# Kernel optimization log

Measured on AMD Instinct MI355X. Metric: run time of the kernel, lower is better.

Reference implementation:

```python
import math
import jax, jax.numpy as jnp
import numpy as np

B, T, G, E, H, L = 8, 32, 32, 768, 12, 4
S = T * G
HD = E // H


def setup_inputs() -> dict:
    key = jax.random.key(0)
    ks = jax.random.split(key, 10)
    def n(k, shape, s=0.02):
        return s * jax.random.normal(k, shape, jnp.float32)
    return dict(
        x=jax.random.normal(ks[0], (B, T, G, E), jnp.float32),
        study_date=jnp.sort(jax.random.randint(ks[1], (B, T), 0, 50), axis=-1),
        wpe=n(ks[2], (50, E)),
        ln1_w=jnp.ones((L, E)), ln1_b=jnp.zeros((L, E)),
        in_w=n(ks[3], (L, 3 * E, E)), in_b=jnp.zeros((L, 3 * E)),
        out_w=n(ks[4], (L, E, E)), out_b=jnp.zeros((L, E)),
        ln2_w=jnp.ones((L, E)), ln2_b=jnp.zeros((L, E)),
        fc_w=n(ks[5], (L, 4 * E, E)), fc_b=jnp.zeros((L, 4 * E)),
        proj_w=n(ks[6], (L, E, 4 * E), 0.02 / math.sqrt(2 * L)),
        proj_b=jnp.zeros((L, E)),
        lnf_w=jnp.ones((E,)), lnf_b=jnp.zeros((E,)),
    )


def _ln(x, w, b):
    m = x.mean(-1, keepdims=True)
    v = ((x - m) ** 2).mean(-1, keepdims=True)
    return (x - m) / jnp.sqrt(v + 1e-5) * w + b


def _gelu_new(x):
    # NewGELU: 0.5*x*(1+tanh(sqrt(2/pi)*(x+0.044715*x^3)))
    c = np.sqrt(2.0 / np.pi).astype(np.float32)
    return 0.5 * x * (1.0 + jnp.tanh(c * (x + 0.044715 * x ** 3)))


def _mask_bias():
    # block-causal mask: tril over T blocks, each expanded to G x G
    allowed = jnp.tril(jnp.ones((T, T), bool))
    allowed = jnp.repeat(jnp.repeat(allowed, G, axis=0), G, axis=1)  # [S,S]
    return jnp.where(allowed, 0.0, -jnp.inf).astype(jnp.float32)


def reference(x, study_date, wpe, ln1_w, ln1_b, in_w, in_b, out_w, out_b,
              ln2_w, ln2_b, fc_w, fc_b, proj_w, proj_b, lnf_w, lnf_b):
    b, t, g, d = x.shape
    s = t * g
    pos = wpe[jnp.clip(study_date, 0, 49)]  # [B,T,E]
    pos = jnp.broadcast_to(pos[:, :, None, :], (b, t, g, d)).reshape(b, s, d)
    h = x.reshape(b, s, d) + pos
    bias = _mask_bias()  # [S,S]
    inv_sqrt_hd = 1.0 / np.sqrt(HD).astype(np.float32)
    for l in range(L):
        y = _ln(h, ln1_w[l], ln1_b[l])
        qkv = y @ in_w[l].T + in_b[l]  # [B,S,3E]
        q, k, v = jnp.split(qkv, 3, axis=-1)
        q = q.reshape(b, s, H, HD).transpose(0, 2, 1, 3)
        k = k.reshape(b, s, H, HD).transpose(0, 2, 1, 3)
        v = v.reshape(b, s, H, HD).transpose(0, 2, 1, 3)
        att = jnp.einsum('bhqd,bhkd->bhqk', q, k) * inv_sqrt_hd + bias
        att = jax.nn.softmax(att, axis=-1)
        o = jnp.einsum('bhqk,bhkd->bhqd', att, v)
        o = o.transpose(0, 2, 1, 3).reshape(b, s, d)
        h = h + o @ out_w[l].T + out_b[l]
        y2 = _ln(h, ln2_w[l], ln2_b[l])
        h = h + _gelu_new(y2 @ fc_w[l].T + fc_b[l]) @ proj_w[l].T + proj_b[l]
    return _ln(h, lnf_w, lnf_b)
```

## Files before the change

### kernel.cpp

```cpp
#include <hip/hip_runtime.h>
#include <hip/hip_bf16.h>

typedef __attribute__((ext_vector_type(8))) __bf16 bf16x8;
typedef __attribute__((ext_vector_type(4))) float f32x4;

typedef unsigned short u16;
typedef __attribute__((ext_vector_type(8))) u16 u16x8;

__device__ __forceinline__ u16 f2bf(float f) {
    unsigned int u = __float_as_uint(f);
    u += 0x7FFFu + ((u >> 16) & 1u);
    return (u16)(u >> 16);
}

__device__ __forceinline__ void g2l16(const void* g, void* l) {
    __builtin_amdgcn_global_load_lds(
        (const __attribute__((address_space(1))) void*)g,
        (__attribute__((address_space(3))) void*)l, 16, 0, 0);
}

#define BB 8
#define SS 1024
#define EE 768
#define HH 12
#define HD 64
#define LL 4

__global__ __launch_bounds__(256) void cvt_k(const float* __restrict__ in,
                                             u16* __restrict__ out, int n4) {
    for (int i = blockIdx.x * 256 + threadIdx.x; i < n4; i += gridDim.x * 256) {
        float4 v = ((const float4*)in)[i];
        ushort4 u;
        u.x = f2bf(v.x); u.y = f2bf(v.y); u.z = f2bf(v.z); u.w = f2bf(v.w);
        ((ushort4*)out)[i] = u;
    }
}

__global__ __launch_bounds__(256) void embed_k(const float* __restrict__ x,
                                               const int* __restrict__ sd,
                                               const float* __restrict__ wpe,
                                               float* __restrict__ h) {
    int idx = blockIdx.x * 256 + threadIdx.x;
    int e4 = idx % 192;
    int bs = idx / 192;
    int b = bs >> 10;
    int t = (bs >> 5) & 31;
    int date = sd[b * 32 + t];
    date = date < 0 ? 0 : (date > 49 ? 49 : date);
    float4 xv = ((const float4*)x)[idx];
    float4 pv = ((const float4*)wpe)[date * 192 + e4];
    float4 r; r.x = xv.x + pv.x; r.y = xv.y + pv.y; r.z = xv.z + pv.z; r.w = xv.w + pv.w;
    ((float4*)h)[idx] = r;
}

template <bool BF16OUT>
__global__ __launch_bounds__(256) void ln_k(const float* __restrict__ in,
                                            const float* __restrict__ w,
                                            const float* __restrict__ b,
                                            void* __restrict__ out) {
    int tid = threadIdx.x, wv = tid >> 6, lane = tid & 63;
    int token = blockIdx.x * 4 + wv;
    const float4* ip = (const float4*)(in + (size_t)token * EE);
    float4 v[3];
#pragma unroll
    for (int p = 0; p < 3; p++) v[p] = ip[p * 64 + lane];
    float s = 0.f;
#pragma unroll
    for (int p = 0; p < 3; p++) s += v[p].x + v[p].y + v[p].z + v[p].w;
#pragma unroll
    for (int m = 1; m < 64; m <<= 1) s += __shfl_xor(s, m);
    float mean = s * (1.f / 768.f);
    float vs = 0.f;
#pragma unroll
    for (int p = 0; p < 3; p++) {
        float dx = v[p].x - mean, dy = v[p].y - mean, dz = v[p].z - mean, dw = v[p].w - mean;
        vs += dx * dx + dy * dy + dz * dz + dw * dw;
    }
#pragma unroll
    for (int m = 1; m < 64; m <<= 1) vs += __shfl_xor(vs, m);
    float rstd = rsqrtf(vs * (1.f / 768.f) + 1e-5f);
    const float4* wp = (const float4*)w;
    const float4* bp = (const float4*)b;
#pragma unroll
    for (int p = 0; p < 3; p++) {
        float4 wv4 = wp[p * 64 + lane], bv4 = bp[p * 64 + lane];
        float rx = (v[p].x - mean) * rstd * wv4.x + bv4.x;
        float ry = (v[p].y - mean) * rstd * wv4.y + bv4.y;
        float rz = (v[p].z - mean) * rstd * wv4.z + bv4.z;
        float rw = (v[p].w - mean) * rstd * wv4.w + bv4.w;
        if (BF16OUT) {
            ushort4 u; u.x = f2bf(rx); u.y = f2bf(ry); u.z = f2bf(rz); u.w = f2bf(rw);
            ((ushort4*)((u16*)out + (size_t)token * EE))[p * 64 + lane] = u;
        } else {
            float4 r; r.x = rx; r.y = ry; r.z = rz; r.w = rw;
            ((float4*)((float*)out + (size_t)token * EE))[p * 64 + lane] = r;
        }
    }
}

template <int MODE, int BM, int NST>
__global__ __launch_bounds__(256) void gemm_bt(const u16* __restrict__ A,
                                               const u16* __restrict__ Bw,
                                               const float* __restrict__ bias,
                                               float* __restrict__ hres,
                                               u16* __restrict__ outb,
                                               u16* __restrict__ vT,
                                               u16* __restrict__ kT,
                                               int M, int N, int K) {
    constexpr int TM = BM / 32;
    constexpr int PD = NST - 2;
    constexpr int ATILE = BM * 32;
    constexpr int TILE = ATILE + 4096;
    constexpr int SSTR = TILE * 2;
    __shared__ u16 SM[NST * TILE];

    const int tid = threadIdx.x;
    const int lane = tid & 63, w = tid >> 6;
    const int quad = lane >> 4, l16 = lane & 15;

    const int nx = N >> 7;
    const int ny = M / BM;
    const int id = blockIdx.x;
    const int xcd = id & 7, s = id >> 3;
    const int yt = xcd * (ny >> 3) + s / nx;
    const int xt = s % nx;
    const int m0 = yt * BM, n0 = xt * 128;
    const int wm = (w >> 1) * (BM / 2), wn = (w & 1) * 64;

    f32x4 acc[TM][4];
#pragma unroll
    for (int i = 0; i < TM; i++)
#pragma unroll
        for (int j = 0; j < 4; j++) acc[i][j] = (f32x4){0.f, 0.f, 0.f, 0.f};

    const int swz = (quad ^ ((l16 >> 1) & 3)) * 8;
    const int nk = K >> 5;

    const int cB0 = w * 128 + lane, cB1 = cB0 + 64;
    const int rB0 = cB0 >> 2, gB0 = (((cB0 & 3) ^ ((cB0 >> 3) & 3)) * 8);
    const int rB1 = cB1 >> 2, gB1 = (((cB1 & 3) ^ ((cB1 >> 3) & 3)) * 8);
    const u16* Bp0 = Bw + (size_t)(n0 + rB0) * K + gB0;
    const u16* Bp1 = Bw + (size_t)(n0 + rB1) * K + gB1;
    char* lB0 = (char*)SM + ATILE * 2 + w * 2048;
    char* lB1 = lB0 + 1024;
    const int cA0 = (BM == 128) ? cB0 : tid;
    const int rA0 = cA0 >> 2, gA0 = (((cA0 & 3) ^ ((cA0 >> 3) & 3)) * 8);
    const u16* Ap0 = A + (size_t)(m0 + rA0) * K + gA0;
    char* lA0 = (char*)SM + ((BM == 128) ? w * 2048 : w * 1024);
    const int cA1 = cB1;
    const int rA1 = cA1 >> 2, gA1 = (((cA1 & 3) ^ ((cA1 >> 3) & 3)) * 8);
    const u16* Ap1 = A + (size_t)(m0 + rA1) * K + gA1;
    char* lA1 = (char*)SM + w * 2048 + 1024;

#pragma unroll
    for (int p = 0; p < PD; p++) {
        g2l16(Ap0 + p * 32, lA0 + p * SSTR);
        if (BM == 128) g2l16(Ap1 + p * 32, lA1 + p * SSTR);
        g2l16(Bp0 + p * 32, lB0 + p * SSTR);
        g2l16(Bp1 + p * 32, lB1 + p * SSTR);
    }

    int rb = 0, wb = PD;
    for (int ki = 0; ki < nk; ki++) {
        if (ki + PD < nk) {
            const int kb = (ki + PD) << 5;
            const int bo = wb * SSTR;
            g2l16(Ap0 + kb, lA0 + bo);
            if (BM == 128) g2l16(Ap1 + kb, lA1 + bo);
            g2l16(Bp0 + kb, lB0 + bo);
            g2l16(Bp1 + kb, lB1 + bo);
        }
        {
            const int rem = nk - 1 - ki;
            const int d = rem < PD ? rem : PD;
            if (BM == 128) {
                if (PD == 2) {
                    if (d == 2)      __builtin_amdgcn_s_waitcnt(0x0F78);
                    else if (d == 1) __builtin_amdgcn_s_waitcnt(0x0F74);
                    else             __builtin_amdgcn_s_waitcnt(0x0F70);
                } else {
                    if (d == 1)      __builtin_amdgcn_s_waitcnt(0x0F74);
                    else             __builtin_amdgcn_s_waitcnt(0x0F70);
                }
            } else {
                if (d == 2)      __builtin_amdgcn_s_waitcnt(0x0F76);
                else if (d == 1) __builtin_amdgcn_s_waitcnt(0x0F73);
                else             __builtin_amdgcn_s_waitcnt(0x0F70);
            }
        }
        __builtin_amdgcn_s_barrier();

        const u16* Ab = (const u16*)SM + rb * TILE;
        const u16* Bb = Ab + ATILE;
        bf16x8 af[TM], bfr[4];
#pragma unroll
        for (int t = 0; t < TM; t++)
            af[t] = *(const bf16x8*)(Ab + (wm + t * 16 + l16) * 32 + swz);
#pragma unroll
        for (int t = 0; t < 4; t++)
            bfr[t] = *(const bf16x8*)(Bb + (wn + t * 16 + l16) * 32 + swz);
#pragma unroll
        for (int tm = 0; tm < TM; tm++)
#pragma unroll
            for (int tn = 0; tn < 4; tn++)
                acc[tm][tn] = __builtin_amdgcn_mfma_f32_16x16x32_bf16(
                    af[tm], bfr[tn], acc[tm][tn], 0, 0, 0);
        rb = (rb + 1 == NST) ? 0 : rb + 1;
        wb = (wb + 1 == NST) ? 0 : wb + 1;
    }

#pragma unroll
    for (int tm = 0; tm < TM; tm++) {
        int rowm = m0 + wm + tm * 16 + quad * 4;
#pragma unroll
        for (int tn = 0; tn < 4; tn++) {
            int coln = n0 + wn + tn * 16 + l16;
            float bv = bias[coln];
            f32x4 v = acc[tm][tn];
            if (MODE == 0) {
                int b = rowm >> 10, s2 = rowm & 1023;
                if (coln < EE) {
                    int hh = coln >> 6, d = coln & 63;
                    u16* qp = outb + ((size_t)(b * HH + hh) * SS + s2) * HD + d;
#pragma unroll
                    for (int r = 0; r < 4; r++) qp[r * HD] = f2bf(v[r] + bv);
                } else if (coln < 2 * EE) {
                    int hh = (coln - EE) >> 6, d = (coln - EE) & 63;
                    u16* kp = kT + ((size_t)(b * HH + hh) * SS + s2) * HD + d;
#pragma unroll
                    for (int r = 0; r < 4; r++) kp[r * HD] = f2bf(v[r] + bv);
                } else {
                    int hh = (coln - 2 * EE) >> 6, d = (coln - 2 * EE) & 63;
                    int j0 = s2 & 31;
                    int k0 = (j0 < 16) ? ((j0 >> 2) * 8) : (((j0 - 16) >> 2) * 8 + 4);
                    int s2p = (s2 & ~31) | k0;
                    ushort4 pk;
                    pk.x = f2bf(v[0] + bv); pk.y = f2bf(v[1] + bv);
                    pk.z = f2bf(v[2] + bv); pk.w = f2bf(v[3] + bv);
                    *(ushort4*)(vT + (((size_t)((b * HH + hh) * HD + d)) << 10) + s2p) = pk;
                }
            } else if (MODE == 1) {
#pragma unroll
                for (int r = 0; r < 4; r++) {
                    size_t idx = (size_t)(rowm + r) * N + coln;
                    hres[idx] += v[r] + bv;
                }
            } else {
#pragma unroll
                for (int r = 0; r < 4; r++) {
                    float x = v[r] + bv;
                    float t = x + 0.044715f * x * x * x;
                    float e = __expf(-1.5957691216057308f * t);
                    float th = (1.f - e) / (1.f + e);
                    outb[(size_t)(rowm + r) * N + coln] = f2bf(0.5f * x * (1.f + th));
                }
            }
        }
    }
}

__global__ __launch_bounds__(256) void attn_k(const u16* __restrict__ qT,
                                              const u16* __restrict__ kT,
                                              const u16* __restrict__ vT,
                                              u16* __restrict__ o) {
    __shared__ u16 Ks[2048];
    __shared__ u16 Vs[2048];
    int tid = threadIdx.x, w = tid >> 6, lane = tid & 63;
    int quad = lane >> 4, l16 = lane & 15;
    int blk = blockIdx.x;
    int qg = 15 - (blk / 96);
    int bh = blk % 96;
    int b = bh / HH, hh = bh % HH;
    int q0 = qg * 64;
    int kend_blk = q0 + 64;
    int kend_w = q0 + ((w >> 1) ? 64 : 32);

    const u16* qbase = qT + ((size_t)bh * SS + q0 + w * 16 + l16) * HD + quad * 8;
    bf16x8 qf0 = *(const bf16x8*)(qbase);
    bf16x8 qf1 = *(const bf16x8*)(qbase + 32);

    f32x4 of[4];
#pragma unroll
    for (int i = 0; i < 4; i++) of[i] = (f32x4){0.f, 0.f, 0.f, 0.f};
    float mrun = -__builtin_inff(), lrun = 0.f;

    int tK = tid >> 3, dcK = ((tid & 7) ^ (tK & 7));
    const u16* kg = kT + ((size_t)bh * SS + tK) * HD + dcK * 8;
    char* kl = (char*)Ks + w * 1024;
    int dV = tid >> 2, tcV = ((tid & 3) ^ ((dV >> 1) & 3));
    const u16* vg = vT + ((size_t)bh * HD + dV) * SS + tcV * 8;
    char* vl = (char*)Vs + w * 1024;

    for (int kb = 0; kb < kend_blk; kb += 32) {
        g2l16(kg + (size_t)kb * HD, kl);
        g2l16(vg + kb, vl);
        __syncthreads();
        if (kb < kend_w) {
            int t0 = l16, t1 = 16 + l16;
            bf16x8 k00 = *(const bf16x8*)(Ks + (t0 * 8 + (quad ^ (l16 & 7))) * 8);
            bf16x8 k01 = *(const bf16x8*)(Ks + (t0 * 8 + ((4 + quad) ^ (l16 & 7))) * 8);
            bf16x8 k10 = *(const bf16x8*)(Ks + (t1 * 8 + (quad ^ (l16 & 7))) * 8);
            bf16x8 k11 = *(const bf16x8*)(Ks + (t1 * 8 + ((4 + quad) ^ (l16 & 7))) * 8);
            f32x4 sT0 = (f32x4){0.f, 0.f, 0.f, 0.f};
            f32x4 sT1 = (f32x4){0.f, 0.f, 0.f, 0.f};
            sT0 = __builtin_amdgcn_mfma_f32_16x16x32_bf16(k00, qf0, sT0, 0, 0, 0);
            sT0 = __builtin_amdgcn_mfma_f32_16x16x32_bf16(k01, qf1, sT0, 0, 0, 0);
            sT1 = __builtin_amdgcn_mfma_f32_16x16x32_bf16(k10, qf0, sT1, 0, 0, 0);
            sT1 = __builtin_amdgcn_mfma_f32_16x16x32_bf16(k11, qf1, sT1, 0, 0, 0);

            float a0[4], a1[4];
#pragma unroll
            for (int r = 0; r < 4; r++) { a0[r] = sT0[r] * 0.125f; a1[r] = sT1[r] * 0.125f; }
            float mx = fmaxf(fmaxf(fmaxf(a0[0], a0[1]), fmaxf(a0[2], a0[3])),
                             fmaxf(fmaxf(a1[0], a1[1]), fmaxf(a1[2], a1[3])));
            mx = fmaxf(mx, __shfl_xor(mx, 16));
            mx = fmaxf(mx, __shfl_xor(mx, 32));
            if (!__all(mx - mrun <= 8.0f)) {
                float mnew = fmaxf(mrun, mx);
                float alpha = __expf(mrun - mnew);
                mrun = mnew;
                lrun *= alpha;
                float al[4];
#pragma unroll
                for (int r = 0; r < 4; r++) al[r] = __shfl(alpha, quad * 4 + r);
#pragma unroll
                for (int n4 = 0; n4 < 4; n4++) {
                    of[n4][0] *= al[0]; of[n4][1] *= al[1];
                    of[n4][2] *= al[2]; of[n4][3] *= al[3];
                }
            }
            float p0[4], p1[4];
#pragma unroll
            for (int r = 0; r < 4; r++) {
                p0[r] = __expf(a0[r] - mrun);
                p1[r] = __expf(a1[r] - mrun);
            }
            float ps = ((p0[0] + p0[1]) + (p0[2] + p0[3])) +
                       ((p1[0] + p1[1]) + (p1[2] + p1[3]));
            ps += __shfl_xor(ps, 16);
            ps += __shfl_xor(ps, 32);
            lrun += ps;
            union { u16x8 u; bf16x8 v; } pa;
            pa.u[0] = f2bf(p0[0]); pa.u[1] = f2bf(p0[1]);
            pa.u[2] = f2bf(p0[2]); pa.u[3] = f2bf(p0[3]);
            pa.u[4] = f2bf(p1[0]); pa.u[5] = f2bf(p1[1]);
            pa.u[6] = f2bf(p1[2]); pa.u[7] = f2bf(p1[3]);
#pragma unroll
            for (int n4 = 0; n4 < 4; n4++) {
                int d = n4 * 16 + l16;
                bf16x8 vf = *(const bf16x8*)(Vs + (d * 4 + (quad ^ ((d >> 1) & 3))) * 8);
                of[n4] = __builtin_amdgcn_mfma_f32_16x16x32_bf16(pa.v, vf, of[n4], 0, 0, 0);
            }
        }
        __syncthreads();
    }

    float linv[4];
#pragma unroll
    for (int r = 0; r < 4; r++) linv[r] = 1.f / __shfl(lrun, quad * 4 + r);
#pragma unroll
    for (int n4 = 0; n4 < 4; n4++)
#pragma unroll
        for (int r = 0; r < 4; r++)
            o[(size_t)(b * SS + q0 + w * 16 + quad * 4 + r) * EE + hh * HD + n4 * 16 + l16] =
                f2bf(of[n4][r] * linv[r]);
}

extern "C" void kernel_launch(void* const* d_in, const int* in_sizes, int n_in,
                              void* d_out, int out_size, void* d_ws, size_t ws_size,
                              hipStream_t stream) {
    const float* x     = (const float*)d_in[0];
    const int*   sd    = (const int*)d_in[1];
    const float* wpe   = (const float*)d_in[2];
    const float* ln1w  = (const float*)d_in[3];
    const float* ln1b  = (const float*)d_in[4];
    const float* in_w  = (const float*)d_in[5];
    const float* in_b  = (const float*)d_in[6];
    const float* out_w = (const float*)d_in[7];
    const float* out_b = (const float*)d_in[8];
    const float* ln2w  = (const float*)d_in[9];
    const float* ln2b  = (const float*)d_in[10];
    const float* fc_w  = (const float*)d_in[11];
    const float* fc_b  = (const float*)d_in[12];
    const float* pr_w  = (const float*)d_in[13];
    const float* pr_b  = (const float*)d_in[14];
    const float* lnfw  = (const float*)d_in[15];
    const float* lnfb  = (const float*)d_in[16];
    float* outp = (float*)d_out;

    char* ws = (char*)d_ws;
    float* h   = (float*)ws;
    u16* ybuf  = (u16*)(ws + 25165824);
    u16* big   = (u16*)(ws + 37748736);
    u16* qT    = big;
    u16* kT    = big + 6291456;
    u16* vT    = (u16*)(ws + 88080384);
    u16* wb    = (u16*)(ws + 100663296);
    u16* w_in  = wb;
    u16* w_out = w_in + 7077888;
    u16* w_fc  = w_out + 2359296;
    u16* w_pr  = w_fc + 9437184;

    cvt_k<<<1024, 256, 0, stream>>>(in_w,  w_in,  7077888 / 4);
    cvt_k<<<1024, 256, 0, stream>>>(out_w, w_out, 2359296 / 4);
    cvt_k<<<1024, 256, 0, stream>>>(fc_w,  w_fc,  9437184 / 4);
    cvt_k<<<1024, 256, 0, stream>>>(pr_w,  w_pr,  9437184 / 4);
    embed_k<<<6144, 256, 0, stream>>>(x, sd, wpe, h);

    for (int l = 0; l < LL; l++) {
        ln_k<true><<<2048, 256, 0, stream>>>(h, ln1w + l * EE, ln1b + l * EE, ybuf);
        gemm_bt<0, 128, 3><<<18 * 64, 256, 0, stream>>>(
            ybuf, w_in + (size_t)l * 2304 * 768, in_b + l * 2304, nullptr, qT, vT, kT,
            8192, 2304, 768);
        attn_k<<<1536, 256, 0, stream>>>(qT, kT, vT, ybuf);
        gemm_bt<1, 64, 4><<<6 * 128, 256, 0, stream>>>(
            ybuf, w_out + (size_t)l * 768 * 768, out_b + l * 768, h, nullptr, nullptr, nullptr,
            8192, 768, 768);
        ln_k<true><<<2048, 256, 0, stream>>>(h, ln2w + l * EE, ln2b + l * EE, ybuf);
        gemm_bt<2, 128, 3><<<24 * 64, 256, 0, stream>>>(
            ybuf, w_fc + (size_t)l * 3072 * 768, fc_b + l * 3072, nullptr, big, nullptr, nullptr,
            8192, 3072, 768);
        gemm_bt<1, 128, 4><<<6 * 64, 256, 0, stream>>>(
            big, w_pr + (size_t)l * 768 * 3072, pr_b + l * 768, h, nullptr, nullptr, nullptr,
            8192, 768, 3072);
    }
    ln_k<false><<<2048, 256, 0, stream>>>(h, lnfw, lnfb, outp);
}
```

Measured before the change: 1.170 ms.

## Split-K the MLP projection GEMM and fold residual add into LayerNorm

The projection GEMM (K=3072) now runs with split-K of 2, doubling the grid from 384 to 768 blocks to fill more CUs. Each half writes its partial sum as bf16 into a scratch buffer (ybuf or vT) instead of doing a read-modify-write on the fp32 residual. The next LayerNorm (or the final one) loads both partials, adds them to h, writes h back and then normalizes, which fuses the residual update into an existing pass. The cost is that the partial sums are rounded to bf16 before accumulation, which loses some precision, and the pipeline depth drops from 4 to 3 stages.

```diff
diff --git a/kernel.cpp b/kernel.cpp
--- a/kernel.cpp
+++ b/kernel.cpp
@@ -11,6 +11,10 @@
     unsigned int u = __float_as_uint(f);
     u += 0x7FFFu + ((u >> 16) & 1u);
     return (u16)(u >> 16);
+}
+
+__device__ __forceinline__ float b2f(u16 u) {
+    return __uint_as_float((unsigned int)u << 16);
 }
 
 __device__ __forceinline__ void g2l16(const void* g, void* l) {
@@ -53,17 +57,37 @@
     ((float4*)h)[idx] = r;
 }
 
-template <bool BF16OUT>
+template <bool BF16OUT, bool ADDP>
 __global__ __launch_bounds__(256) void ln_k(const float* __restrict__ in,
                                             const float* __restrict__ w,
                                             const float* __restrict__ b,
-                                            void* __restrict__ out) {
+                                            void* __restrict__ out,
+                                            const u16* p0, const u16* p1,
+                                            float* hback) {
     int tid = threadIdx.x, wv = tid >> 6, lane = tid & 63;
     int token = blockIdx.x * 4 + wv;
     const float4* ip = (const float4*)(in + (size_t)token * EE);
     float4 v[3];
 #pragma unroll
     for (int p = 0; p < 3; p++) v[p] = ip[p * 64 + lane];
+    if (ADDP) {
+        const ushort4* q0 = (const ushort4*)(p0 + (size_t)token * EE);
+        const ushort4* q1 = (const ushort4*)(p1 + (size_t)token * EE);
+#pragma unroll
+        for (int p = 0; p < 3; p++) {
+            ushort4 a = q0[p * 64 + lane];
+            ushort4 c = q1[p * 64 + lane];
+            v[p].x += b2f(a.x) + b2f(c.x);
+            v[p].y += b2f(a.y) + b2f(c.y);
+            v[p].z += b2f(a.z) + b2f(c.z);
+            v[p].w += b2f(a.w) + b2f(c.w);
+        }
+        if (hback) {
+            float4* hp = (float4*)(hback + (size_t)token * EE);
+#pragma unroll
+            for (int p = 0; p < 3; p++) hp[p * 64 + lane] = v[p];
+        }
+    }
     float s = 0.f;
 #pragma unroll
     for (int p = 0; p < 3; p++) s += v[p].x + v[p].y + v[p].z + v[p].w;
@@ -98,7 +122,7 @@
     }
 }
 
-template <int MODE, int BM, int NST>
+template <int MODE, int BM, int NST, int SPLITK>
 __global__ __launch_bounds__(256) void gemm_bt(const u16* __restrict__ A,
                                                const u16* __restrict__ Bw,
                                                const float* __restrict__ bias,
@@ -120,12 +144,19 @@
 
     const int nx = N >> 7;
     const int ny = M / BM;
-    const int id = blockIdx.x;
+    int id = blockIdx.x;
+    int ks = 0;
+    if (SPLITK == 2) {
+        const int half = ny * nx;
+        ks = id >= half;
+        id -= ks * half;
+    }
     const int xcd = id & 7, s = id >> 3;
     const int yt = xcd * (ny >> 3) + s / nx;
     const int xt = s % nx;
     const int m0 = yt * BM, n0 = xt * 128;
     const int wm = (w >> 1) * (BM / 2), wn = (w & 1) * 64;
+    const int kbase = ks * (K / SPLITK);
 
     f32x4 acc[TM][4];
 #pragma unroll
@@ -134,22 +165,22 @@
         for (int j = 0; j < 4; j++) acc[i][j] = (f32x4){0.f, 0.f, 0.f, 0.f};
 
     const int swz = (quad ^ ((l16 >> 1) & 3)) * 8;
-    const int nk = K >> 5;
+    const int nk = (K / SPLITK) >> 5;
 
     const int cB0 = w * 128 + lane, cB1 = cB0 + 64;
     const int rB0 = cB0 >> 2, gB0 = (((cB0 & 3) ^ ((cB0 >> 3) & 3)) * 8);
     const int rB1 = cB1 >> 2, gB1 = (((cB1 & 3) ^ ((cB1 >> 3) & 3)) * 8);
-    const u16* Bp0 = Bw + (size_t)(n0 + rB0) * K + gB0;
-    const u16* Bp1 = Bw + (size_t)(n0 + rB1) * K + gB1;
+    const u16* Bp0 = Bw + (size_t)(n0 + rB0) * K + kbase + gB0;
+    const u16* Bp1 = Bw + (size_t)(n0 + rB1) * K + kbase + gB1;
     char* lB0 = (char*)SM + ATILE * 2 + w * 2048;
     char* lB1 = lB0 + 1024;
     const int cA0 = (BM == 128) ? cB0 : tid;
     const int rA0 = cA0 >> 2, gA0 = (((cA0 & 3) ^ ((cA0 >> 3) & 3)) * 8);
-    const u16* Ap0 = A + (size_t)(m0 + rA0) * K + gA0;
+    const u16* Ap0 = A + (size_t)(m0 + rA0) * K + kbase + gA0;
     char* lA0 = (char*)SM + ((BM == 128) ? w * 2048 : w * 1024);
     const int cA1 = cB1;
     const int rA1 = cA1 >> 2, gA1 = (((cA1 & 3) ^ ((cA1 >> 3) & 3)) * 8);
-    const u16* Ap1 = A + (size_t)(m0 + rA1) * K + gA1;
+    const u16* Ap1 = A + (size_t)(m0 + rA1) * K + kbase + gA1;
     char* lA1 = (char*)SM + w * 2048 + 1024;
 
 #pragma unroll
@@ -245,7 +276,7 @@
                     size_t idx = (size_t)(rowm + r) * N + coln;
                     hres[idx] += v[r] + bv;
                 }
-            } else {
+            } else if (MODE == 2) {
 #pragma unroll
                 for (int r = 0; r < 4; r++) {
                     float x = v[r] + bv;
@@ -254,6 +285,12 @@
                     float th = (1.f - e) / (1.f + e);
                     outb[(size_t)(rowm + r) * N + coln] = f2bf(0.5f * x * (1.f + th));
                 }
+            } else {
+                u16* pb = ks ? vT : outb;
+                float badd = ks ? 0.f : bv;
+#pragma unroll
+                for (int r = 0; r < 4; r++)
+                    pb[(size_t)(rowm + r) * N + coln] = f2bf(v[r] + badd);
             }
         }
     }
@@ -408,21 +445,28 @@
     embed_k<<<6144, 256, 0, stream>>>(x, sd, wpe, h);
 
     for (int l = 0; l < LL; l++) {
-        ln_k<true><<<2048, 256, 0, stream>>>(h, ln1w + l * EE, ln1b + l * EE, ybuf);
-        gemm_bt<0, 128, 3><<<18 * 64, 256, 0, stream>>>(
+        if (l == 0)
+            ln_k<true, false><<<2048, 256, 0, stream>>>(
+                h, ln1w + l * EE, ln1b + l * EE, ybuf, nullptr, nullptr, nullptr);
+        else
+            ln_k<true, true><<<2048, 256, 0, stream>>>(
+                h, ln1w + l * EE, ln1b + l * EE, ybuf, ybuf, vT, h);
+        gemm_bt<0, 128, 3, 1><<<18 * 64, 256, 0, stream>>>(
             ybuf, w_in + (size_t)l * 2304 * 768, in_b + l * 2304, nullptr, qT, vT, kT,
             8192, 2304, 768);
         attn_k<<<1536, 256, 0, stream>>>(qT, kT, vT, ybuf);
-        gemm_bt<1, 64, 4><<<6 * 128, 256, 0, stream>>>(
+        gemm_bt<1, 64, 4, 1><<<6 * 128, 256, 0, stream>>>(
             ybuf, w_out + (size_t)l * 768 * 768, out_b + l * 768, h, nullptr, nullptr, nullptr,
             8192, 768, 768);
-        ln_k<true><<<2048, 256, 0, stream>>>(h, ln2w + l * EE, ln2b + l * EE, ybuf);
-        gemm_bt<2, 128, 3><<<24 * 64, 256, 0, stream>>>(
+        ln_k<true, false><<<2048, 256, 0, stream>>>(
+            h, ln2w + l * EE, ln2b + l * EE, ybuf, nullptr, nullptr, nullptr);
+        gemm_bt<2, 128, 3, 1><<<24 * 64, 256, 0, stream>>>(
             ybuf, w_fc + (size_t)l * 3072 * 768, fc_b + l * 3072, nullptr, big, nullptr, nullptr,
             8192, 3072, 768);
-        gemm_bt<1, 128, 4><<<6 * 64, 256, 0, stream>>>(
-            big, w_pr + (size_t)l * 768 * 3072, pr_b + l * 768, h, nullptr, nullptr, nullptr,
+        gemm_bt<3, 128, 3, 2><<<2 * 6 * 64, 256, 0, stream>>>(
+            big, w_pr + (size_t)l * 768 * 3072, pr_b + l * 768, nullptr, ybuf, vT, nullptr,
             8192, 768, 3072);
     }
-    ln_k<false><<<2048, 256, 0, stream>>>(h, lnfw, lnfb, outp);
-}
+    ln_k<false, true><<<2048, 256, 0, stream>>>(
+        h, lnfw, lnfb, outp, ybuf, vT, nullptr);
+}
```

New measurement: 1.134 ms. 1.03x faster.
